# Kernel optimization log

Hardware: AMD Instinct MI355X
Metric: run time of the kernel (lower is better)

## Reference

```python
import jax, jax.numpy as jnp
import numpy as np

N = 100000
E = 1600000
D_IN = 128
D_HID = 128

def setup_inputs() -> dict:
    key = jax.random.key(0)
    ks = jax.random.split(key, 8)
    x = jax.random.normal(ks[0], (N, D_IN), dtype=jnp.float32)
    edge_index = jax.random.randint(ks[1], (2, E), 0, N, dtype=jnp.int32)
    edge_weight = jax.random.uniform(ks[2], (E,), dtype=jnp.float32)
    W1 = jax.random.normal(ks[3], (D_IN, D_HID), dtype=jnp.float32) / np.sqrt(D_IN)
    b1 = jnp.zeros((D_HID,), dtype=jnp.float32)
    W2 = jax.random.normal(ks[4], (D_HID, D_HID), dtype=jnp.float32) / np.sqrt(D_HID)
    b2 = jnp.zeros((D_HID,), dtype=jnp.float32)
    W3 = jax.random.normal(ks[5], (D_HID, 1), dtype=jnp.float32) / np.sqrt(D_HID)
    b3 = jnp.zeros((1,), dtype=jnp.float32)
    return {"x": x, "edge_index": edge_index, "edge_weight": edge_weight,
            "W1": W1, "b1": b1, "W2": W2, "b2": b2, "W3": W3, "b3": b3}

def _gcn_norm(edge_index, edge_weight, n):
    # Add self-loops (weight 1) and compute symmetric normalization, as in PyG GCNConv.
    loop = jnp.arange(n, dtype=edge_index.dtype)
    src = jnp.concatenate([edge_index[0], loop])
    dst = jnp.concatenate([edge_index[1], loop])
    w = jnp.concatenate([edge_weight, jnp.ones((n,), edge_weight.dtype)])
    deg = jax.ops.segment_sum(w, dst, num_segments=n)  # [N]
    dis = jnp.where(deg > 0, jax.lax.rsqrt(jnp.where(deg > 0, deg, 1.0)), 0.0)
    norm = dis[src] * w * dis[dst]  # [E+N]
    return src, dst, norm

def _gcn_conv(x, W, b, src, dst, norm, n):
    h = x @ W  # [N, out]
    msg = norm[:, None] * h[src]  # gather + scale, [E+N, out]
    out = jax.ops.segment_sum(msg, dst, num_segments=n)  # scatter-add
    return out + b

def reference(x, edge_index, edge_weight, W1, b1, W2, b2, W3, b3):
    n = x.shape[0]
    src, dst, norm = _gcn_norm(edge_index, edge_weight, n)
    h = jax.nn.relu(_gcn_conv(x, W1, b1, src, dst, norm, n))
    h = jax.nn.relu(_gcn_conv(h, W2, b2, src, dst, norm, n))
    h = _gcn_conv(h, W3, b3, src, dst, norm, n)
    return jax.nn.relu(h).squeeze(-1)  # [N]
```

## Files before the change

### kernel.cpp

```cpp
#include <hip/hip_runtime.h>
#include <hip/hip_fp16.h>
#include <math.h>

#define NFEAT 128
#define CAP 64

typedef int2 EdgeRec;

__device__ inline float4 h4_to_f4(uint2 u) {
  __half2 lo = *(__half2*)&u.x;
  __half2 hi = *(__half2*)&u.y;
  float2 a = __half22float2(lo), b = __half22float2(hi);
  return make_float4(a.x, a.y, b.x, b.y);
}
__device__ inline uint2 f4_to_h4(float4 v) {
  __half2 lo = __floats2half2_rn(v.x, v.y);
  __half2 hi = __floats2half2_rn(v.z, v.w);
  uint2 r; r.x = *(unsigned*)&lo; r.y = *(unsigned*)&hi; return r;
}

__global__ __launch_bounds__(256) void k_build(const int* __restrict__ src,
                                               const int* __restrict__ dst,
                                               const float* __restrict__ ew,
                                               unsigned* __restrict__ cnt,
                                               EdgeRec* __restrict__ ep, int E) {
  int i = blockIdx.x * blockDim.x + threadIdx.x;
  int stride = gridDim.x * blockDim.x;
  for (int e = i; e < E; e += stride) {
    int d = dst[e];
    int s = src[e];
    float w = ew[e];
    unsigned slot = atomicAdd(&cnt[d], 1u);
    EdgeRec r; r.x = s; r.y = __float_as_int(w);
    ep[(size_t)d * CAP + slot] = r;
  }
}

__global__ __launch_bounds__(256) void k_dis(const unsigned* __restrict__ cnt,
                                             const EdgeRec* __restrict__ ep,
                                             float* __restrict__ dis, int N) {
  int wave = threadIdx.x >> 6;
  int lane = threadIdx.x & 63;
  int node = blockIdx.x * 4 + wave;
  if (node >= N) return;
  int c = (int)cnt[node];
  float w = 0.f;
  if (lane < c) w = __int_as_float(ep[node * CAP + lane].y);
#pragma unroll
  for (int off = 32; off > 0; off >>= 1) w += __shfl_down(w, off, 64);
  if (lane == 0) dis[node] = 1.0f / sqrtf(1.0f + w);
}

__global__ __launch_bounds__(256) void k_premul(EdgeRec* __restrict__ ep,
                                                const unsigned* __restrict__ cnt,
                                                const float* __restrict__ dis, int N) {
  int wave = threadIdx.x >> 6;
  int lane = threadIdx.x & 63;
  int node = blockIdx.x * 4 + wave;
  if (node >= N) return;
  int c = (int)cnt[node];
  if (lane < c) {
    int e = node * CAP + lane;
    EdgeRec r = ep[e];
    r.y = __float_as_int(dis[r.x] * __int_as_float(r.y));
    ep[e] = r;
  }
}


__global__ __launch_bounds__(1024) void k_gemm1(const float* __restrict__ X,
                                                const float* __restrict__ W,
                                                __half* __restrict__ Y,
                                                int N, int numTiles) {
  __shared__ float sW[128 * 128];
  __shared__ float sX[128 * 128];
  int t = threadIdx.x;
  int wave = __builtin_amdgcn_readfirstlane(t >> 6);
  int lane = t & 63;
  int lr = (lane >> 3) & 7;
  int lc = lane & 7;
  int wr = wave >> 2;
  int wc = wave & 3;

  {
    const float4* W4 = (const float4*)W;
    float4* sW4 = (float4*)sW;
    for (int i = t; i < 4096; i += 1024) sW4[i] = W4[i];
  }

  const float4* X4 = (const float4*)X;
  int grmax = N - 1;
  int r0 = wr * 32 + lr * 4;
  int c0 = wc * 32 + lc * 4;
  int swzk = ((r0 >> 2) & 7) << 2;

  for (int tile = blockIdx.x; tile < numTiles; tile += gridDim.x) {
    int rowBase = tile * 128;
    __syncthreads();
    {
      int kg = t & 31;
      int rb = t >> 5;
#pragma unroll
      for (int p = 0; p < 4; p++) {
        int r = rb + 32 * p;
        int gr = rowBase + r; if (gr > grmax) gr = grmax;
        float4 v = X4[(size_t)gr * 32 + kg];
        int swz = ((r >> 2) & 7) << 2;
        *(float4*)(&sX[r * 128 + ((kg * 4) ^ swz)]) = v;
      }
    }
    __syncthreads();

    float4 acc[4];
#pragma unroll
    for (int i = 0; i < 4; i++) acc[i] = make_float4(0.f, 0.f, 0.f, 0.f);

#pragma unroll 1
    for (int kg = 0; kg < 32; kg++) {
      int kk0 = kg * 4;
      float4 xf[4];
#pragma unroll
      for (int i = 0; i < 4; i++)
        xf[i] = *(const float4*)(&sX[(r0 + i) * 128 + (kk0 ^ swzk)]);
      float4 wf[4];
#pragma unroll
      for (int kk = 0; kk < 4; kk++)
        wf[kk] = *(const float4*)(&sW[(kk0 + kk) * 128 + c0]);
#pragma unroll
      for (int kk = 0; kk < 4; kk++) {
#pragma unroll
        for (int i = 0; i < 4; i++) {
          float xs = (&xf[i].x)[kk];
          acc[i].x = fmaf(xs, wf[kk].x, acc[i].x);
          acc[i].y = fmaf(xs, wf[kk].y, acc[i].y);
          acc[i].z = fmaf(xs, wf[kk].z, acc[i].z);
          acc[i].w = fmaf(xs, wf[kk].w, acc[i].w);
        }
      }
    }

#pragma unroll
    for (int i = 0; i < 4; i++) {
      int row = rowBase + r0 + i;
      if (row < N)
        *(uint2*)(Y + (size_t)row * 128 + c0) = f4_to_h4(acc[i]);
    }
  }
}


__global__ __launch_bounds__(1024) void k_aggemm(const __half* __restrict__ H,
                                                 const unsigned* __restrict__ cntA,
                                                 const EdgeRec* __restrict__ ep,
                                                 const float* __restrict__ dis,
                                                 const float* __restrict__ bias,
                                                 const float* __restrict__ Wm,
                                                 __half* __restrict__ Y,
                                                 int N, int numTiles) {
  __shared__ float sW[128 * 128];
  __shared__ float sX[2][64 * 128];
  int t = threadIdx.x;
  int wave = __builtin_amdgcn_readfirstlane(t >> 6);
  int lane = t & 63;

  {
    const float4* W4 = (const float4*)Wm;
    float4* sW4 = (float4*)sW;
    for (int i = t; i < 4096; i += 1024) sW4[i] = W4[i];
  }
  __syncthreads();

  int gw = wave;
  int half = lane >> 5;
  int l32 = lane & 31;
  int mw = wave - 12;
  int wr = (mw >> 1) & 1;
  int wc = mw & 1;
  int lr = (lane >> 3) & 7;
  int lc = lane & 7;
  int rB = wr * 32 + lr * 4;
  int cA = wc * 64 + lc * 4;
  int cB = cA + 32;
  int swzm = lr << 2;
  int s2b = 2 * gw;

  for (int it = 0;; it++) {
    int gtile = blockIdx.x + it * gridDim.x;
    int mtile = gtile - (int)gridDim.x;
    bool anyG = gtile < numTiles;
    bool anyM = (it >= 1) && (mtile < numTiles);
    if (!anyG && !anyM) break;

    if (wave < 12) {
      if (anyG) {
        float* buf = sX[it & 1];
        int tileBase = gtile * 64;
        int cnts[3];
#pragma unroll
        for (int k = 0; k < 3; k++) {
          int s2 = s2b + 24 * k;
          int node = tileBase + s2 + half;
          int nodec = node < N ? node : N - 1;
          unsigned pk = cntA[nodec];
          cnts[k] = (s2 < 64 && node < N) ? (int)pk : 0;
        }
#pragma unroll 1
        for (int k = 0; k < 3; k++) {
          int s2 = s2b + 24 * k;
          if (s2 >= 64) break;
          int node = tileBase + s2 + half;
          int cnt = cnts[k];
          int beg = (node < N ? node : 0) * CAP;
          int last = beg + cnt - 1;

          float4 acc = make_float4(0.f, 0.f, 0.f, 0.f);
          if (cnt > 0) {
            EdgeRec e0[4], e1[4], e2[4], e3[4];
            uint2 h0[4], h1[4];
#pragma unroll
            for (int q = 0; q < 4; q++) { int e = beg + q;     e0[q] = ep[e <= last ? e : last]; }
#pragma unroll
            for (int q = 0; q < 4; q++) { int e = beg + 4 + q; e1[q] = ep[e <= last ? e : last]; }
#pragma unroll
            for (int q = 0; q < 4; q++) { int e = beg + 8 + q; e2[q] = ep[e <= last ? e : last]; }
#pragma unroll
            for (int q = 0; q < 4; q++)
              h0[q] = *(const uint2*)(H + (size_t)e0[q].x * 128 + 4 * l32);
#pragma unroll
            for (int q = 0; q < 4; q++)
              h1[q] = *(const uint2*)(H + (size_t)e1[q].x * 128 + 4 * l32);
            for (int p = 0; p < cnt; p += 4) {
              uint2 h2[4];
#pragma unroll
              for (int q = 0; q < 4; q++) {
                int e = beg + p + 12 + q;
                e3[q] = ep[e <= last ? e : last];
              }
#pragma unroll
              for (int q = 0; q < 4; q++)
                h2[q] = *(const uint2*)(H + (size_t)e2[q].x * 128 + 4 * l32);
#pragma unroll
              for (int q = 0; q < 4; q++) {
                float w = (p + q < cnt) ? __int_as_float(e0[q].y) : 0.f;
                float4 hv = h4_to_f4(h0[q]);
                acc.x = fmaf(w, hv.x, acc.x);
                acc.y = fmaf(w, hv.y, acc.y);
                acc.z = fmaf(w, hv.z, acc.z);
                acc.w = fmaf(w, hv.w, acc.w);
              }
#pragma unroll
              for (int q = 0; q < 4; q++) {
                e0[q] = e1[q]; e1[q] = e2[q]; e2[q] = e3[q];
                h0[q] = h1[q]; h1[q] = h2[q];
              }
            }
          }
          if (node < N) {
            float ds = dis[node];
            float4 hn = h4_to_f4(*(const uint2*)(H + (size_t)node * 128 + 4 * l32));
            acc.x = fmaf(ds, hn.x, acc.x);
            acc.y = fmaf(ds, hn.y, acc.y);
            acc.z = fmaf(ds, hn.z, acc.z);
            acc.w = fmaf(ds, hn.w, acc.w);
            float4 bv = *(const float4*)(bias + 4 * l32);
            float4 o;
            o.x = fmaf(ds, acc.x, bv.x); o.x = o.x > 0.f ? o.x : 0.f;
            o.y = fmaf(ds, acc.y, bv.y); o.y = o.y > 0.f ? o.y : 0.f;
            o.z = fmaf(ds, acc.z, bv.z); o.z = o.z > 0.f ? o.z : 0.f;
            o.w = fmaf(ds, acc.w, bv.w); o.w = o.w > 0.f ? o.w : 0.f;
            int s = s2 + half;
            int swz = ((s >> 2) & 7) << 2;
            *(float4*)(&buf[s * 128 + ((4 * l32) ^ swz)]) = o;
          }
        }
      }
    } else {
      if (anyM) {
        const float* buf = sX[(it - 1) & 1];
        float4 accA[4], accB[4];
#pragma unroll
        for (int i = 0; i < 4; i++) {
          accA[i] = make_float4(0.f, 0.f, 0.f, 0.f);
          accB[i] = make_float4(0.f, 0.f, 0.f, 0.f);
        }
#pragma unroll 2
        for (int kg = 0; kg < 32; kg++) {
          int kk0 = kg * 4;
          float4 xf[4];
#pragma unroll
          for (int i = 0; i < 4; i++)
            xf[i] = *(const float4*)(&buf[(rB + i) * 128 + (kk0 ^ swzm)]);
#pragma unroll
          for (int kk = 0; kk < 4; kk++) {
            float4 wA = *(const float4*)(&sW[(kk0 + kk) * 128 + cA]);
            float4 wB = *(const float4*)(&sW[(kk0 + kk) * 128 + cB]);
#pragma unroll
            for (int i = 0; i < 4; i++) {
              float xs = (&xf[i].x)[kk];
              accA[i].x = fmaf(xs, wA.x, accA[i].x);
              accA[i].y = fmaf(xs, wA.y, accA[i].y);
              accA[i].z = fmaf(xs, wA.z, accA[i].z);
              accA[i].w = fmaf(xs, wA.w, accA[i].w);
              accB[i].x = fmaf(xs, wB.x, accB[i].x);
              accB[i].y = fmaf(xs, wB.y, accB[i].y);
              accB[i].z = fmaf(xs, wB.z, accB[i].z);
              accB[i].w = fmaf(xs, wB.w, accB[i].w);
            }
          }
        }
        int rowBase = mtile * 64;
#pragma unroll
        for (int i = 0; i < 4; i++) {
          int row = rowBase + rB + i;
          if (row < N) {
            *(uint2*)(Y + (size_t)row * 128 + cA) = f4_to_h4(accA[i]);
            *(uint2*)(Y + (size_t)row * 128 + cB) = f4_to_h4(accB[i]);
          }
        }
      }
    }
    __syncthreads();
  }
}


__global__ __launch_bounds__(256) void k_agg_final(const __half* __restrict__ H,
                                                   const unsigned* __restrict__ cntA,
                                                   const EdgeRec* __restrict__ ep,
                                                   const float* __restrict__ dis,
                                                   const float* __restrict__ bias,
                                                   const float* __restrict__ W3,
                                                   float* __restrict__ z, int N) {
  int wave = __builtin_amdgcn_readfirstlane(threadIdx.x >> 6);
  int lane = threadIdx.x & 63;
  int half = lane >> 5;
  int l32  = lane & 31;
  int node = blockIdx.x * 8 + wave * 2 + half;
  int nodec = node < N ? node : N - 1;
  int cnt = (node < N) ? (int)cntA[nodec] : 0;
  int beg = nodec * CAP;
  int last = beg + cnt - 1;

  float4 acc = make_float4(0.f, 0.f, 0.f, 0.f);
  if (cnt > 0) {
    EdgeRec e0[4], e1[4], e2[4];
    uint2 h0[4], h1[4];
#pragma unroll
    for (int q = 0; q < 4; q++) { int e = beg + q;     e0[q] = ep[e <= last ? e : last]; }
#pragma unroll
    for (int q = 0; q < 4; q++) { int e = beg + 4 + q; e1[q] = ep[e <= last ? e : last]; }
#pragma unroll
    for (int q = 0; q < 4; q++)
      h0[q] = *(const uint2*)(H + (size_t)e0[q].x * 128 + 4 * l32);
    for (int p = 0; p < cnt; p += 4) {
      uint2 h1n[4];
#pragma unroll
      for (int q = 0; q < 4; q++) {
        int e = beg + p + 8 + q;
        e2[q] = ep[e <= last ? e : last];
      }
#pragma unroll
      for (int q = 0; q < 4; q++)
        h1n[q] = *(const uint2*)(H + (size_t)e1[q].x * 128 + 4 * l32);
#pragma unroll
      for (int q = 0; q < 4; q++) {
        float w = (p + q < cnt) ? __int_as_float(e0[q].y) : 0.f;
        float4 hv = h4_to_f4(h0[q]);
        acc.x = fmaf(w, hv.x, acc.x);
        acc.y = fmaf(w, hv.y, acc.y);
        acc.z = fmaf(w, hv.z, acc.z);
        acc.w = fmaf(w, hv.w, acc.w);
      }
#pragma unroll
      for (int q = 0; q < 4; q++) { e0[q] = e1[q]; e1[q] = e2[q]; h0[q] = h1n[q]; }
    }
  }
  float ds = dis[nodec];
  float4 hn = h4_to_f4(*(const uint2*)(H + (size_t)nodec * 128 + 4 * l32));
  acc.x = fmaf(ds, hn.x, acc.x);
  acc.y = fmaf(ds, hn.y, acc.y);
  acc.z = fmaf(ds, hn.z, acc.z);
  acc.w = fmaf(ds, hn.w, acc.w);
  float4 bv = *(const float4*)(bias + 4 * l32);
  float4 w3v = *(const float4*)(W3 + 4 * l32);
  float o, pdot = 0.f;
  o = fmaf(ds, acc.x, bv.x); o = o > 0.f ? o : 0.f; pdot = fmaf(o, w3v.x, pdot);
  o = fmaf(ds, acc.y, bv.y); o = o > 0.f ? o : 0.f; pdot = fmaf(o, w3v.y, pdot);
  o = fmaf(ds, acc.z, bv.z); o = o > 0.f ? o : 0.f; pdot = fmaf(o, w3v.z, pdot);
  o = fmaf(ds, acc.w, bv.w); o = o > 0.f ? o : 0.f; pdot = fmaf(o, w3v.w, pdot);
#pragma unroll
  for (int off = 16; off > 0; off >>= 1) pdot += __shfl_down(pdot, off, 32);
  if (l32 == 0 && node < N) z[node] = pdot;
}


__global__ void k_aggs(const float* __restrict__ z, const unsigned* __restrict__ cntA,
                       const EdgeRec* __restrict__ ep, const float* __restrict__ dis,
                       const float* __restrict__ b3, float* __restrict__ out, int N) {
  int n = blockIdx.x * blockDim.x + threadIdx.x;
  if (n >= N) return;
  int cnt = (int)cntA[n];
  float dsn = dis[n];
  float acc = dsn * z[n];
  int beg = n * CAP;
#pragma unroll 4
  for (int e = beg; e < beg + cnt; e++) {
    EdgeRec p = ep[e];
    acc = fmaf(__int_as_float(p.y), z[p.x], acc);
  }
  acc = fmaf(dsn, acc, b3[0]);
  out[n] = acc > 0.f ? acc : 0.f;
}


extern "C" void kernel_launch(void* const* d_in, const int* in_sizes, int n_in,
                              void* d_out, int out_size, void* d_ws, size_t ws_size,
                              hipStream_t stream) {
  const float* x  = (const float*)d_in[0];
  const int*   ei = (const int*)d_in[1];
  const float* ew = (const float*)d_in[2];
  const float* W1 = (const float*)d_in[3];
  const float* b1 = (const float*)d_in[4];
  const float* W2 = (const float*)d_in[5];
  const float* b2 = (const float*)d_in[6];
  const float* W3 = (const float*)d_in[7];
  const float* b3 = (const float*)d_in[8];
  int N = in_sizes[0] / NFEAT;
  int E = in_sizes[2];
  const int* srcp = ei;
  const int* dstp = ei + E;

  char* p = (char*)d_ws;
  auto carve = [&](size_t bytes) -> void* {
    void* r = (void*)p;
    p += (bytes + 511) & ~(size_t)511;
    return r;
  };
  unsigned* cnt = (unsigned*)carve(sizeof(unsigned) * N);
  float*   dis = (float*)carve(sizeof(float) * N);
  EdgeRec* ep  = (EdgeRec*)carve(sizeof(EdgeRec) * (size_t)N * CAP);
  __half*  t1  = (__half*)carve(sizeof(__half) * (size_t)N * NFEAT);
  __half*  t2  = (__half*)carve(sizeof(__half) * (size_t)N * NFEAT);
  float*   z   = (float*)carve(sizeof(float) * N);

  int gN = (N + 255) / 256;
  int numTiles128 = (N + 127) / 128;
  int numTiles64  = (N + 63) / 64;
  int GG = 256;
  int gB = 2048;
  int gP = (N + 3) / 4;
  int gF = (N + 7) / 8;

  hipMemsetAsync(cnt, 0, sizeof(unsigned) * N, stream);
  k_build<<<gB, 256, 0, stream>>>(srcp, dstp, ew, cnt, ep, E);
  k_gemm1<<<GG, 1024, 0, stream>>>(x, W1, t1, N, numTiles128);
  k_dis<<<gP, 256, 0, stream>>>(cnt, ep, dis, N);
  k_premul<<<gP, 256, 0, stream>>>(ep, cnt, dis, N);
  k_aggemm<<<GG, 1024, 0, stream>>>(t1, cnt, ep, dis, b1, W2, t2, N, numTiles64);
  k_agg_final<<<gF, 256, 0, stream>>>(t2, cnt, ep, dis, b2, W3, z, N);
  k_aggs<<<gN, 256, 0, stream>>>(z, cnt, ep, dis, b3, (float*)d_out, N);
}
```

Before: 494.2 us.

## Build adjacency via two-level binned counting sort instead of global atomics

Replaces the single global-atomic edge bucketing kernel with a histogram, scan, scatter and per-bin CSR pass. Destination-bin counting happens in shared memory, and the final per-node slot assignment and degree sums are done with LDS atomics inside one block per 128-node bin. The per-node degree reduction kernel is folded into the CSR pass. This adds three extra launches, a single-block serial scan and an extra pass over a sorted edge buffer. Packing 24-bit source ids assumes N fits in 24 bits.

```diff
diff --git a/kernel.cpp b/kernel.cpp
--- a/kernel.cpp
+++ b/kernel.cpp
@@ -4,6 +4,8 @@
 
 #define NFEAT 128
 #define CAP 64
+#define BINSHIFT 7
+#define GB 256
 
 typedef int2 EdgeRec;
 
@@ -19,36 +21,106 @@
   uint2 r; r.x = *(unsigned*)&lo; r.y = *(unsigned*)&hi; return r;
 }
 
-__global__ __launch_bounds__(256) void k_build(const int* __restrict__ src,
-                                               const int* __restrict__ dst,
-                                               const float* __restrict__ ew,
-                                               unsigned* __restrict__ cnt,
-                                               EdgeRec* __restrict__ ep, int E) {
-  int i = blockIdx.x * blockDim.x + threadIdx.x;
-  int stride = gridDim.x * blockDim.x;
-  for (int e = i; e < E; e += stride) {
+
+__global__ __launch_bounds__(256) void k_hist(const int* __restrict__ dst,
+                                              unsigned* __restrict__ histG,
+                                              int E, int EPB, int nbins) {
+  __shared__ unsigned lh[1024];
+  for (int i = threadIdx.x; i < nbins; i += 256) lh[i] = 0;
+  __syncthreads();
+  int start = blockIdx.x * EPB;
+  int end = start + EPB; if (end > E) end = E;
+  for (int e = start + threadIdx.x; e < end; e += 256)
+    atomicAdd(&lh[dst[e] >> BINSHIFT], 1u);
+  __syncthreads();
+  for (int i = threadIdx.x; i < nbins; i += 256)
+    histG[(size_t)blockIdx.x * nbins + i] = lh[i];
+}
+
+__global__ __launch_bounds__(1024) void k_scan(unsigned* __restrict__ histG,
+                                               unsigned* __restrict__ binBase,
+                                               int nbins) {
+  __shared__ unsigned tot[1024];
+  int b = threadIdx.x;
+  unsigned running = 0;
+  if (b < nbins)
+    for (int blk = 0; blk < GB; blk++) running += histG[(size_t)blk * nbins + b];
+  tot[b] = (b < nbins) ? running : 0;
+  __syncthreads();
+  for (int off = 1; off < 1024; off <<= 1) {
+    unsigned v = (b >= off) ? tot[b - off] : 0;
+    __syncthreads();
+    tot[b] += v;
+    __syncthreads();
+  }
+  unsigned base = (b == 0) ? 0u : tot[b - 1];
+  if (b < nbins) binBase[b] = base;
+  if (b == 0) binBase[nbins] = tot[1023];
+  if (b < nbins) {
+    unsigned run = base;
+    for (int blk = 0; blk < GB; blk++) {
+      unsigned v = histG[(size_t)blk * nbins + b];
+      histG[(size_t)blk * nbins + b] = run;
+      run += v;
+    }
+  }
+}
+
+__global__ __launch_bounds__(256) void k_scatter(const int* __restrict__ src,
+                                                 const int* __restrict__ dst,
+                                                 const float* __restrict__ ew,
+                                                 const unsigned* __restrict__ histG,
+                                                 uint2* __restrict__ sorted,
+                                                 int E, int EPB, int nbins) {
+  __shared__ unsigned lrank[1024];
+  __shared__ unsigned lbase[1024];
+  for (int i = threadIdx.x; i < nbins; i += 256) {
+    lrank[i] = 0;
+    lbase[i] = histG[(size_t)blockIdx.x * nbins + i];
+  }
+  __syncthreads();
+  int start = blockIdx.x * EPB;
+  int end = start + EPB; if (end > E) end = E;
+  for (int e = start + threadIdx.x; e < end; e += 256) {
     int d = dst[e];
-    int s = src[e];
-    float w = ew[e];
-    unsigned slot = atomicAdd(&cnt[d], 1u);
-    EdgeRec r; r.x = s; r.y = __float_as_int(w);
-    ep[(size_t)d * CAP + slot] = r;
-  }
-}
-
-__global__ __launch_bounds__(256) void k_dis(const unsigned* __restrict__ cnt,
-                                             const EdgeRec* __restrict__ ep,
+    int bin = d >> BINSHIFT;
+    unsigned r = atomicAdd(&lrank[bin], 1u);
+    uint2 rec;
+    rec.x = (unsigned)src[e] | ((unsigned)(d & 127) << 24);
+    rec.y = __float_as_uint(ew[e]);
+    sorted[lbase[bin] + r] = rec;
+  }
+}
+
+__global__ __launch_bounds__(256) void k_csr(const uint2* __restrict__ sorted,
+                                             const unsigned* __restrict__ binBase,
+                                             unsigned* __restrict__ cnt,
+                                             EdgeRec* __restrict__ ep,
                                              float* __restrict__ dis, int N) {
-  int wave = threadIdx.x >> 6;
-  int lane = threadIdx.x & 63;
-  int node = blockIdx.x * 4 + wave;
-  if (node >= N) return;
-  int c = (int)cnt[node];
-  float w = 0.f;
-  if (lane < c) w = __int_as_float(ep[node * CAP + lane].y);
-#pragma unroll
-  for (int off = 32; off > 0; off >>= 1) w += __shfl_down(w, off, 64);
-  if (lane == 0) dis[node] = 1.0f / sqrtf(1.0f + w);
+  int bin = blockIdx.x;
+  __shared__ unsigned lcnt[128];
+  __shared__ float lsum[128];
+  if (threadIdx.x < 128) { lcnt[threadIdx.x] = 0; lsum[threadIdx.x] = 0.f; }
+  __syncthreads();
+  unsigned s0 = binBase[bin], s1 = binBase[bin + 1];
+  int node0 = bin << BINSHIFT;
+  for (unsigned e = s0 + threadIdx.x; e < s1; e += 256) {
+    uint2 rec = sorted[e];
+    int dlow = rec.x >> 24;
+    int srcn = rec.x & 0xFFFFFF;
+    unsigned slot = atomicAdd(&lcnt[dlow], 1u);
+    EdgeRec r; r.x = srcn; r.y = (int)rec.y;
+    ep[(size_t)(node0 + dlow) * CAP + slot] = r;
+    atomicAdd(&lsum[dlow], __uint_as_float(rec.y));
+  }
+  __syncthreads();
+  if (threadIdx.x < 128) {
+    int node = node0 + threadIdx.x;
+    if (node < N) {
+      cnt[node] = lcnt[threadIdx.x];
+      dis[node] = 1.0f / sqrtf(1.0f + lsum[threadIdx.x]);
+    }
+  }
 }
 
 __global__ __launch_bounds__(256) void k_premul(EdgeRec* __restrict__ ep,
@@ -436,25 +508,30 @@
     p += (bytes + 511) & ~(size_t)511;
     return r;
   };
-  unsigned* cnt = (unsigned*)carve(sizeof(unsigned) * N);
-  float*   dis = (float*)carve(sizeof(float) * N);
-  EdgeRec* ep  = (EdgeRec*)carve(sizeof(EdgeRec) * (size_t)N * CAP);
-  __half*  t1  = (__half*)carve(sizeof(__half) * (size_t)N * NFEAT);
-  __half*  t2  = (__half*)carve(sizeof(__half) * (size_t)N * NFEAT);
-  float*   z   = (float*)carve(sizeof(float) * N);
+  int nbins = (N + 127) >> BINSHIFT;
+  unsigned* cnt     = (unsigned*)carve(sizeof(unsigned) * N);
+  float*    dis     = (float*)carve(sizeof(float) * N);
+  EdgeRec*  ep      = (EdgeRec*)carve(sizeof(EdgeRec) * (size_t)N * CAP);
+  __half*   t1      = (__half*)carve(sizeof(__half) * (size_t)N * NFEAT);
+  __half*   t2      = (__half*)carve(sizeof(__half) * (size_t)N * NFEAT);
+  float*    z       = (float*)carve(sizeof(float) * N);
+  unsigned* histG   = (unsigned*)carve(sizeof(unsigned) * (size_t)GB * nbins);
+  unsigned* binBase = (unsigned*)carve(sizeof(unsigned) * (nbins + 1));
+  uint2*    sorted  = (uint2*)carve(sizeof(uint2) * (size_t)E);
 
   int gN = (N + 255) / 256;
   int numTiles128 = (N + 127) / 128;
   int numTiles64  = (N + 63) / 64;
   int GG = 256;
-  int gB = 2048;
+  int EPB = (E + GB - 1) / GB;
   int gP = (N + 3) / 4;
   int gF = (N + 7) / 8;
 
-  hipMemsetAsync(cnt, 0, sizeof(unsigned) * N, stream);
-  k_build<<<gB, 256, 0, stream>>>(srcp, dstp, ew, cnt, ep, E);
+  k_hist<<<GB, 256, 0, stream>>>(dstp, histG, E, EPB, nbins);
+  k_scan<<<1, 1024, 0, stream>>>(histG, binBase, nbins);
+  k_scatter<<<GB, 256, 0, stream>>>(srcp, dstp, ew, histG, sorted, E, EPB, nbins);
+  k_csr<<<nbins, 256, 0, stream>>>(sorted, binBase, cnt, ep, dis, N);
   k_gemm1<<<GG, 1024, 0, stream>>>(x, W1, t1, N, numTiles128);
-  k_dis<<<gP, 256, 0, stream>>>(cnt, ep, dis, N);
   k_premul<<<gP, 256, 0, stream>>>(ep, cnt, dis, N);
   k_aggemm<<<GG, 1024, 0, stream>>>(t1, cnt, ep, dis, b1, W2, t2, N, numTiles64);
   k_agg_final<<<gF, 256, 0, stream>>>(t2, cnt, ep, dis, b2, W3, z, N);
```

After: 473.0 us. 4.3% less time.
